# Optimization experiments

Hardware: AMD Instinct MI355X
Metric: run time of the kernel (lower is better)

The kernel has to match this reference:

```python
import jax, jax.numpy as jnp
import numpy as np
import math

B, T, D, CAP = 4, 1024, 512, 32768
MEM_UPDATE_MOMENTUM = 0.99
MEM_NEW_DATA_RATE = 0.01

def setup_inputs() -> dict:
    key = jax.random.key(0)
    k1, k2, k3, k4, k5 = jax.random.split(key, 5)
    keys = jax.random.normal(k1, (B, T, D), dtype=jnp.float32)
    values = jax.random.normal(k2, (B, T, D), dtype=jnp.float32)
    importance = jax.random.uniform(k3, (B, T, 1), dtype=jnp.float32)
    query = jax.random.normal(k4, (B, T, D), dtype=jnp.float32)
    # xavier_uniform on (1, CAP, D): fan_in=D, fan_out=CAP (torch treats dim-1/dim-2)
    bound = math.sqrt(6.0 / (CAP + D))
    mem = jax.random.uniform(k5, (1, CAP, D), minval=-bound, maxval=bound, dtype=jnp.float32)
    return {"keys": keys, "values": values, "importance": importance, "query": query, "mem": mem}

def reference(keys, values, importance, query, mem):
    b, t, d = keys.shape
    cap = mem.shape[1]
    # ---- write ----
    scores = jnp.einsum('btd,ocd->btc', keys, mem)          # [b, t, cap]
    usage = jax.nn.softmax(scores, axis=-1).sum(axis=1)     # [b, cap]
    combined = importance.mean(axis=(1, 2))                 # [b]
    write_priority = combined[:, None] + 0.1 * usage        # [b, cap]
    k = min(t, cap)
    _, indices = jax.lax.top_k(write_priority, k)           # [b, k]
    values_write = values[:, :k]                            # [b, k, d]
    scatter = jnp.zeros((b, cap, d), dtype=keys.dtype)
    scatter = scatter.at[jnp.arange(b)[:, None], indices].set(values_write)
    new_mem = mem * MEM_UPDATE_MOMENTUM + scatter.mean(axis=0, keepdims=True) * MEM_NEW_DATA_RATE
    # ---- read (against updated memory) ----
    attn = jnp.einsum('bqd,ocd->bqc', query, new_mem) / math.sqrt(d)
    attn = jax.nn.softmax(attn, axis=-1)                    # [b, q, cap]
    out = jnp.einsum('bqc,ocd->bqd', attn, new_mem)         # [b, q, d]
    return out
```

## Files before the change

### kernel.cpp

```cpp
#include <hip/hip_runtime.h>

typedef float f32x4 __attribute__((ext_vector_type(4)));
typedef short s16x8 __attribute__((ext_vector_type(8)));
typedef short s16x4 __attribute__((ext_vector_type(4)));
typedef unsigned short ush;

constexpr int Bn = 4, Tn = 1024, Dn = 512, CAPn = 32768, Kn = 1024;
constexpr int ROWS = Bn * Tn;
constexpr float SCALE = 0.044194173824159216f;
constexpr float MOM = 0.99f;
constexpr float RATE_B = 0.0025f;

constexpr size_t OFF_NM    = 0;
constexpr size_t OFF_NMT   = 33554432;
constexpr size_t OFF_OPART = 67108864;
constexpr size_t OFF_KHF   = 67108864;
constexpr size_t OFF_ZPART = 75497472;
constexpr size_t OFF_PRIO  = 83886080;
constexpr size_t OFF_RANK  = 84410368;
constexpr size_t OFF_COMB  = 84934656;
constexpr size_t OFF_ZP2   = 100663296;

#define MFMA(a, b, c) __builtin_amdgcn_mfma_f32_16x16x32_bf16((a), (b), (c), 0, 0, 0)
#define MFMAH(a, b, c) __builtin_amdgcn_mfma_f32_16x16x32_f16((a), (b), (c), 0, 0, 0)

__device__ __forceinline__ ush bfrn(float x) {
  unsigned u = __float_as_uint(x);
  return (ush)((u + 0x7FFFu + ((u >> 16) & 1u)) >> 16);
}
__device__ __forceinline__ float bff(ush h) { return __uint_as_float(((unsigned)h) << 16); }
__device__ __forceinline__ ush f16rn(float x) {
  _Float16 h = (_Float16)x;
  return *(ush*)&h;
}

__device__ __forceinline__ void gl16(const ush* g, ush* l) {
  __builtin_amdgcn_global_load_lds(
      (const __attribute__((address_space(1))) void*)(uintptr_t)g,
      (__attribute__((address_space(3))) void*)(uintptr_t)l, 16, 0, 0);
}

__global__ void k_combined(const float* __restrict__ imp, float* __restrict__ comb) {
  __shared__ float red[256];
  int b = blockIdx.x;
  float s = 0.f;
  for (int t = threadIdx.x; t < Tn; t += 256) s += imp[(size_t)b * Tn + t];
  red[threadIdx.x] = s;
  __syncthreads();
  for (int off = 128; off > 0; off >>= 1) {
    if (threadIdx.x < (unsigned)off) red[threadIdx.x] += red[threadIdx.x + off];
    __syncthreads();
  }
  if (threadIdx.x == 0) comb[b] = red[0] * (1.0f / Tn);
}

__global__ void k_cvt_f16(const float* __restrict__ x, ush* __restrict__ o) {
  size_t i = ((size_t)blockIdx.x * 256 + threadIdx.x) * 4;
  f32x4 v = *(const f32x4*)&x[i];
  s16x4 h;
#pragma unroll
  for (int j = 0; j < 4; ++j) h[j] = (short)f16rn(v[j]);
  *(s16x4*)&o[i] = h;
}

__global__ __launch_bounds__(256, 2) void k_rowexp(const ush* __restrict__ Ahf,
                                                   const ush* __restrict__ Bhf,
                                                   float* __restrict__ zpart) {
  __shared__ ush Bs[64 * 512];
  __shared__ float red[2][64];
  const int tid = threadIdx.x;
  const int lane = tid & 63, wid = tid >> 6;
  const int wc2 = wid >> 1, wt = wid & 1;
  const int l15 = lane & 15, g = lane >> 4;
  const int cb = blockIdx.x;
  const int cBase = cb * 64;

  s16x8 afr[2][16];
#pragma unroll
  for (int mi = 0; mi < 2; ++mi) {
    int c = cBase + wc2 * 32 + mi * 16 + l15;
#pragma unroll
    for (int ks = 0; ks < 16; ++ks)
      afr[mi][ks] = *(const s16x8*)&Ahf[(size_t)c * Dn + ks * 32 + g * 8];
  }

  for (int tt = 0; tt < 64; ++tt) {
    const int tBase = tt * 64;
#pragma unroll
    for (int rr = 0; rr < 16; ++rr) {
      int idx = rr * 256 + tid;
      int row = idx >> 6, ch = idx & 63;
      gl16(&Bhf[(size_t)(tBase + row) * Dn + ((ch ^ (row & 7)) << 3)],
           &Bs[rr * 2048 + wid * 512]);
    }
    __syncthreads();
    f32x4 S[2][2];
#pragma unroll
    for (int mi = 0; mi < 2; ++mi)
#pragma unroll
      for (int ni = 0; ni < 2; ++ni) S[mi][ni] = (f32x4){0.f, 0.f, 0.f, 0.f};
#pragma unroll
    for (int ks = 0; ks < 16; ++ks) {
      s16x8 bfr[2];
#pragma unroll
      for (int ni = 0; ni < 2; ++ni) {
        int trow = wt * 32 + ni * 16 + l15;
        bfr[ni] = *(const s16x8*)&Bs[trow * 512 + (((ks * 4 + g) ^ (trow & 7)) * 8)];
      }
#pragma unroll
      for (int mi = 0; mi < 2; ++mi)
#pragma unroll
        for (int ni = 0; ni < 2; ++ni) S[mi][ni] = MFMAH(afr[mi][ks], bfr[ni], S[mi][ni]);
    }
    float tacc[2] = {0.f, 0.f};
#pragma unroll
    for (int mi = 0; mi < 2; ++mi)
#pragma unroll
      for (int ni = 0; ni < 2; ++ni)
#pragma unroll
        for (int r = 0; r < 4; ++r) tacc[ni] += __expf(S[mi][ni][r]);
#pragma unroll
    for (int ni = 0; ni < 2; ++ni) {
      float v = tacc[ni];
      v += __shfl_xor(v, 16);
      v += __shfl_xor(v, 32);
      tacc[ni] = v;
    }
    if (g == 0) {
      red[wc2][wt * 32 + l15] = tacc[0];
      red[wc2][wt * 32 + 16 + l15] = tacc[1];
    }
    __syncthreads();
    if (tid < 64) zpart[(size_t)cb * ROWS + tBase + tid] = red[0][tid] + red[1][tid];
  }
}

__global__ void k_invl(const float* __restrict__ zpart, float* __restrict__ invl) {
  int t = blockIdx.x * 256 + threadIdx.x;
  float s = 0.f;
  for (int cb = 0; cb < 512; ++cb) s += zpart[(size_t)cb * ROWS + t];
  invl[t] = 1.0f / s;
}

__global__ __launch_bounds__(256, 3) void k_usage(const ush* __restrict__ mhf,
                                                  const ush* __restrict__ khf,
                                                  const float* __restrict__ invl,
                                                  const float* __restrict__ comb,
                                                  float* __restrict__ prio) {
  __shared__ ush Ah[128 * 64], Bh[128 * 64];
  const int tid = threadIdx.x;
  const int lane = tid & 63, w = tid >> 6;
  const int l15 = lane & 15, g = lane >> 4;
  const int cBase = blockIdx.x * 128;
  const int b = blockIdx.y;
  const ush* khb = khf + (size_t)b * Tn * Dn;
  const int r0 = tid >> 3, u0 = tid & 7;
  const int usw = (u0 ^ (r0 & 7)) << 3;

  float uacc[2][4] = {{0.f, 0.f, 0.f, 0.f}, {0.f, 0.f, 0.f, 0.f}};
  for (int tt = 0; tt < 8; ++tt) {
    f32x4 S[2][8];
#pragma unroll
    for (int mi = 0; mi < 2; ++mi)
#pragma unroll
      for (int ni = 0; ni < 8; ++ni) S[mi][ni] = (f32x4){0.f, 0.f, 0.f, 0.f};
    for (int kk = 0; kk < 8; ++kk) {
      __syncthreads();
      {
        size_t a0 = (size_t)(cBase + r0) * Dn + kk * 64 + usw;
        size_t a1 = (size_t)(cBase + r0 + 64) * Dn + kk * 64 + usw;
        gl16(&mhf[a0], &Ah[w * 512]);
        gl16(&mhf[a1], &Ah[4096 + w * 512]);
        size_t b0 = (size_t)(tt * 128 + r0) * Dn + kk * 64 + usw;
        size_t b1 = (size_t)(tt * 128 + r0 + 64) * Dn + kk * 64 + usw;
        gl16(&khb[b0], &Bh[w * 512]);
        gl16(&khb[b1], &Bh[4096 + w * 512]);
      }
      __syncthreads();
#pragma unroll
      for (int ks2 = 0; ks2 < 2; ++ks2) {
        s16x8 ah[2];
#pragma unroll
        for (int mi = 0; mi < 2; ++mi) {
          int crow = w * 32 + mi * 16 + l15;
          ah[mi] = *(const s16x8*)&Ah[crow * 64 + (((ks2 * 4 + g) ^ (crow & 7)) * 8)];
        }
#pragma unroll
        for (int ni = 0; ni < 8; ++ni) {
          int trow = ni * 16 + l15;
          s16x8 bh = *(const s16x8*)&Bh[trow * 64 + (((ks2 * 4 + g) ^ (trow & 7)) * 8)];
#pragma unroll
          for (int mi = 0; mi < 2; ++mi) S[mi][ni] = MFMAH(ah[mi], bh, S[mi][ni]);
        }
      }
    }
#pragma unroll
    for (int ni = 0; ni < 8; ++ni) {
      float il = invl[b * Tn + tt * 128 + ni * 16 + l15];
#pragma unroll
      for (int mi = 0; mi < 2; ++mi)
#pragma unroll
        for (int r = 0; r < 4; ++r) uacc[mi][r] += __expf(S[mi][ni][r]) * il;
    }
  }
#pragma unroll
  for (int mi = 0; mi < 2; ++mi)
#pragma unroll
    for (int r = 0; r < 4; ++r) {
      float v = uacc[mi][r];
      v += __shfl_xor(v, 1);
      v += __shfl_xor(v, 2);
      v += __shfl_xor(v, 4);
      v += __shfl_xor(v, 8);
      if (l15 == 0)
        prio[(size_t)b * CAPn + cBase + w * 32 + mi * 16 + g * 4 + r] =
            comb[b] + 0.1f * v;
    }
}

__global__ void k_rankinit(int* __restrict__ rank) {
  rank[blockIdx.x * 256 + threadIdx.x] = Kn;
}

__global__ __launch_bounds__(1024) void k_select(const float* __restrict__ prio,
                                                 int* __restrict__ rank) {
  const int b = blockIdx.x;
  const float* p = prio + (size_t)b * CAPn;
  __shared__ int hist[256];
  __shared__ unsigned long long s_pref;
  __shared__ int s_krem;
  __shared__ int s_cnt;
  __shared__ unsigned long long selk[Kn];
  const int tid = threadIdx.x;
  if (tid == 0) { s_pref = 0ull; s_krem = Kn; s_cnt = 0; }

#define KEYOF(c, kk)                                                         \
  {                                                                          \
    unsigned mb_ = __float_as_uint(p[(c)]);                                  \
    mb_ = (mb_ & 0x80000000u) ? ~mb_ : (mb_ | 0x80000000u);                  \
    (kk) = ((unsigned long long)mb_ << 32) | (unsigned)(0xFFFFFFFFu - (c));  \
  }

  __syncthreads();
  for (int pos = 56; pos >= 0; pos -= 8) {
    if (tid < 256) hist[tid] = 0;
    __syncthreads();
    unsigned long long pref = s_pref;
    unsigned long long maskhi = (pos == 56) ? 0ull : (~0ull << (pos + 8));
    for (int c = tid; c < CAPn; c += 1024) {
      unsigned long long k;
      KEYOF(c, k);
      if ((k & maskhi) == pref) atomicAdd(&hist[(int)((k >> pos) & 255)], 1);
    }
    __syncthreads();
    if (tid == 0) {
      int krem = s_krem;
      int d = 255;
      for (;; --d) {
        int h = hist[d];
        if (krem <= h || d == 0) break;
        krem -= h;
      }
      s_pref = pref | ((unsigned long long)d << pos);
      s_krem = krem;
    }
    __syncthreads();
  }
  unsigned long long T = s_pref;
  for (int c = tid; c < CAPn; c += 1024) {
    unsigned long long k;
    KEYOF(c, k);
    if (k >= T) {
      int idx = atomicAdd(&s_cnt, 1);
      selk[idx] = k;
    }
  }
  __syncthreads();
  unsigned long long mine = selk[tid];
  int r = 0;
  for (int j = 0; j < Kn; ++j) r += (selk[j] > mine) ? 1 : 0;
  int c = (int)(0xFFFFFFFFu - (unsigned)(mine & 0xFFFFFFFFull));
  rank[(size_t)b * CAPn + c] = r;
#undef KEYOF
}

__global__ void k_newmem(const float* __restrict__ mem, const float* __restrict__ values,
                         const int* __restrict__ rank, ush* __restrict__ nm) {
  int gid = blockIdx.x * 256 + threadIdx.x;
  int c = gid >> 7;
  int q = (gid & 127) << 2;
  f32x4 m = *(const f32x4*)&mem[(size_t)c * Dn + q];
  f32x4 acc = {0.f, 0.f, 0.f, 0.f};
#pragma unroll
  for (int b = 0; b < Bn; ++b) {
    int r = rank[(size_t)b * CAPn + c];
    if (r < Kn) acc += *(const f32x4*)&values[((size_t)b * Tn + r) * Dn + q];
  }
  f32x4 res = m * MOM + acc * RATE_B;
  s16x4 o;
#pragma unroll
  for (int j = 0; j < 4; ++j) o[j] = (short)bfrn(res[j]);
  *(s16x4*)&nm[(size_t)c * Dn + q] = o;
}

__global__ void k_nmT(const ush* __restrict__ nm, ush* __restrict__ nmT) {
  __shared__ ush tile[64][65];
  int cBase = blockIdx.x * 64, dBase = blockIdx.y * 64;
  int tid = threadIdx.x;
#pragma unroll
  for (int rr = 0; rr < 2; ++rr) {
    int idx = rr * 256 + tid;
    int row = idx >> 3, ch = idx & 7;
    s16x8 v = *(const s16x8*)&nm[(size_t)(cBase + row) * Dn + dBase + ch * 8];
#pragma unroll
    for (int j = 0; j < 8; ++j) tile[row][ch * 8 + j] = (ush)v[j];
  }
  __syncthreads();
#pragma unroll
  for (int rr = 0; rr < 2; ++rr) {
    int idx = rr * 256 + tid;
    int drow = idx >> 3, ch = idx & 7;
    s16x8 v;
#pragma unroll
    for (int j = 0; j < 8; ++j) v[j] = (short)tile[ch * 8 + j][drow];
    *(s16x8*)&nmT[(size_t)(dBase + drow) * CAPn + cBase + ch * 8] = v;
  }
}

#define WAITV2 asm volatile("s_waitcnt vmcnt(2)" ::: "memory")
#define WAITL0 asm volatile("s_waitcnt lgkmcnt(0)" ::: "memory")
#define BAR __builtin_amdgcn_s_barrier()
__global__ __launch_bounds__(512, 1) void k_attnout(
    const float* __restrict__ query, const ush* __restrict__ nm,
    const ush* __restrict__ nmT, ush* __restrict__ opart,
    float* __restrict__ zp2) {
  __shared__ ush lds[65536];
  __shared__ float zred[128];
  __shared__ float zacc[128];
  constexpr int LMS = 0, LMT = 24576, LPS = 49152;
  const int tid = threadIdx.x;
  const int lane = tid & 63, w = tid >> 6;
  const int l15 = lane & 15, g = lane >> 4;
  const int cy = blockIdx.x;
  const int qBase = blockIdx.y * 128;
  const int q = w * 16 + l15;
  const int r0 = tid >> 3, u0 = tid & 7;
  const int usw = (u0 ^ (r0 & 7)) << 3;

  auto stage_ms = [&](int buf, int cb_, int kk) {
    const ush* src = nm + (size_t)cb_ * Dn + kk * 64;
    gl16(&src[(size_t)r0 * Dn + usw], &lds[LMS + buf * 8192 + w * 512]);
    gl16(&src[(size_t)(r0 + 64) * Dn + usw], &lds[LMS + buf * 8192 + 4096 + w * 512]);
  };
  auto stage_mt = [&](int buf, int cb_, int u) {
    const ush* src = nmT + (size_t)((u >> 1) * 128) * CAPn + cb_ + (u & 1) * 64;
    gl16(&src[(size_t)r0 * CAPn + usw], &lds[LMT + buf * 8192 + w * 512]);
    gl16(&src[(size_t)(r0 + 64) * CAPn + usw], &lds[LMT + buf * 8192 + 4096 + w * 512]);
  };

  s16x8 qfr[16];
  {
    const float* qsrc = query + (size_t)(qBase + q) * Dn;
#pragma unroll
    for (int ks = 0; ks < 16; ++ks) {
      f32x4 a = *(const f32x4*)&qsrc[ks * 32 + g * 8];
      f32x4 b = *(const f32x4*)&qsrc[ks * 32 + g * 8 + 4];
      s16x8 h;
#pragma unroll
      for (int j = 0; j < 4; ++j) {
        h[j] = (short)bfrn(a[j]);
        h[4 + j] = (short)bfrn(b[j]);
      }
      qfr[ks] = h;
    }
  }

  f32x4 O[32];
#pragma unroll
  for (int i = 0; i < 32; ++i) O[i] = (f32x4){0.f, 0.f, 0.f, 0.f};
  if (tid < 128) zacc[tid] = 0.f;

  stage_ms(0, cy * 4096, 0);
  stage_ms(1, cy * 4096, 1);

  for (int ct = 0; ct < 32; ++ct) {
    const int cBase = cy * 4096 + ct * 128;
    const int cNext = cy * 4096 + ((ct + 1) & 31) * 128;

    f32x4 S[8];
#pragma unroll
    for (int i = 0; i < 8; ++i) S[i] = (f32x4){0.f, 0.f, 0.f, 0.f};
#pragma unroll
    for (int kk = 0; kk < 8; ++kk) {
      WAITV2;
      WAITL0;
      BAR;
      if (kk < 6) stage_ms((kk + 2) % 3, cBase, kk + 2);
      else if (kk == 6) stage_mt(0, cBase, 0);
      else stage_mt(1, cBase, 1);
      __builtin_amdgcn_s_setprio(1);
#pragma unroll
      for (int ks2 = 0; ks2 < 2; ++ks2) {
#pragma unroll
        for (int mi = 0; mi < 8; ++mi) {
          int row = mi * 16 + l15;
          s16x8 am = *(const s16x8*)&lds[LMS + (kk % 3) * 8192 + row * 64 +
                                         (((ks2 * 4 + g) ^ (row & 7)) << 3)];
          S[mi] = MFMA(am, qfr[kk * 2 + ks2], S[mi]);
        }
      }
      __builtin_amdgcn_s_setprio(0);
    }

    float zl = 0.f;
#pragma unroll
    for (int mi = 0; mi < 8; ++mi) {
      s16x4 p;
#pragma unroll
      for (int r = 0; r < 4; ++r) {
        float e = __expf(S[mi][r] * SCALE);
        zl += e;
        p[r] = (short)bfrn(e);
      }
      int u16 = (mi * 2 + (g >> 1)) ^ l15;
      *(s16x4*)&lds[LPS + q * 128 + u16 * 8 + (g & 1) * 4] = p;
    }
    zl += __shfl_xor(zl, 16);
    zl += __shfl_xor(zl, 32);
    if (g == 0) zred[q] = zl;
    WAITL0;
    BAR;
    if (tid < 128) zacc[tid] += zred[tid];

#pragma unroll
    for (int u = 0; u < 8; ++u) {
      WAITV2;
      WAITL0;
      BAR;
      if (u < 6) stage_mt((u + 2) % 3, cBase, u + 2);
      else if (u == 6) stage_ms(0, cNext, 0);
      else stage_ms(1, cNext, 1);
      __builtin_amdgcn_s_setprio(1);
      const int hh = u & 1;
#pragma unroll
      for (int kc = 0; kc < 2; ++kc) {
        int u16 = (hh * 8 + kc * 4 + g) ^ l15;
        s16x8 pb = *(const s16x8*)&lds[LPS + q * 128 + u16 * 8];
#pragma unroll
        for (int mi = 0; mi < 8; ++mi) {
          int row = mi * 16 + l15;
          s16x8 am = *(const s16x8*)&lds[LMT + (u % 3) * 8192 + row * 64 +
                                         (((kc * 4 + g) ^ (row & 7)) << 3)];
          O[(u >> 1) * 8 + mi] = MFMA(am, pb, O[(u >> 1) * 8 + mi]);
        }
      }
      __builtin_amdgcn_s_setprio(0);
    }
  }

  __syncthreads();
  if (tid < 128) zp2[(size_t)cy * ROWS + qBase + tid] = zacc[tid];
#pragma unroll
  for (int ds = 0; ds < 4; ++ds) {
    __syncthreads();
#pragma unroll
    for (int mi = 0; mi < 8; ++mi) {
      s16x4 ov;
#pragma unroll
      for (int r = 0; r < 4; ++r) ov[r] = (short)bfrn(O[ds * 8 + mi][r]);
      int u16 = (mi * 2 + (g >> 1)) ^ l15;
      *(s16x4*)&lds[LPS + q * 128 + u16 * 8 + (g & 1) * 4] = ov;
    }
    __syncthreads();
#pragma unroll
    for (int i = 0; i < 4; ++i) {
      int slot = i * 512 + tid;
      int qq = slot >> 4, u16 = slot & 15;
      s16x8 v = *(const s16x8*)&lds[LPS + qq * 128 + ((u16 ^ (qq & 15)) << 3)];
      *(s16x8*)&opart[((size_t)cy * ROWS + qBase + qq) * Dn + ds * 128 + u16 * 8] = v;
    }
  }
}

__global__ void k_merge(const ush* __restrict__ opart, const float* __restrict__ zp2,
                        float* __restrict__ out) {
  size_t i = ((size_t)blockIdx.x * 256 + threadIdx.x) * 4;
  int row = (int)(i >> 9);
  float z = 0.f;
#pragma unroll
  for (int cyy = 0; cyy < 8; ++cyy) z += zp2[(size_t)cyy * ROWS + row];
  float inv = 1.0f / z;
  f32x4 acc = {0.f, 0.f, 0.f, 0.f};
#pragma unroll
  for (int cyy = 0; cyy < 8; ++cyy) {
    s16x4 a = *(const s16x4*)&opart[(size_t)cyy * ROWS * Dn + i];
#pragma unroll
    for (int j = 0; j < 4; ++j) acc[j] += bff((ush)a[j]);
  }
#pragma unroll
  for (int j = 0; j < 4; ++j) acc[j] *= inv;
  *(f32x4*)&out[i] = acc;
}

extern "C" void kernel_launch(void* const* d_in, const int* in_sizes, int n_in,
                              void* d_out, int out_size, void* d_ws, size_t ws_size,
                              hipStream_t stream) {
  const float* keys = (const float*)d_in[0];
  const float* values = (const float*)d_in[1];
  const float* importance = (const float*)d_in[2];
  const float* query = (const float*)d_in[3];
  const float* mem = (const float*)d_in[4];
  char* wsb = (char*)d_ws;
  ush* nm    = (ush*)(wsb + OFF_NM);
  ush* nmT   = (ush*)(wsb + OFF_NMT);
  ush* mhf   = (ush*)(wsb + OFF_NMT);
  ush* khf   = (ush*)(wsb + OFF_KHF);
  ush* opart = (ush*)(wsb + OFF_OPART);
  float* zpart = (float*)(wsb + OFF_ZPART);
  float* prio  = (float*)(wsb + OFF_PRIO);
  int* rank    = (int*)(wsb + OFF_RANK);
  float* comb  = (float*)(wsb + OFF_COMB);
  float* zp2   = (float*)(wsb + OFF_ZP2);
  float* invl1 = (float*)(wsb + OFF_COMB + 64);
  float* out = (float*)d_out;

  k_combined<<<Bn, 256, 0, stream>>>(importance, comb);
  k_cvt_f16<<<(ROWS * Dn / 4) / 256, 256, 0, stream>>>(keys, khf);
  k_cvt_f16<<<(CAPn * Dn / 4) / 256, 256, 0, stream>>>(mem, mhf);
  k_rowexp<<<CAPn / 64, 256, 0, stream>>>(mhf, khf, zpart);
  k_invl<<<ROWS / 256, 256, 0, stream>>>(zpart, invl1);
  k_usage<<<dim3(CAPn / 128, Bn), 256, 0, stream>>>(mhf, khf, invl1, comb, prio);
  k_rankinit<<<(Bn * CAPn) / 256, 256, 0, stream>>>(rank);
  k_select<<<Bn, 1024, 0, stream>>>(prio, rank);
  k_newmem<<<(CAPn * Dn / 4) / 256, 256, 0, stream>>>(mem, values, rank, nm);
  k_nmT<<<dim3(CAPn / 64, Dn / 64), 256, 0, stream>>>(nm, nmT);
  k_attnout<<<dim3(8, ROWS / 128), 512, 0, stream>>>(query, nm, nmT, opart, zp2);
  k_merge<<<(ROWS * Dn / 4) / 256, 256, 0, stream>>>(opart, zp2, out);
}
```

Before: 959.3 us.

## Use FP8 for the read-score GEMM and fuse new-memory build into transpose

```diff
diff --git a/kernel.cpp b/kernel.cpp
--- a/kernel.cpp
+++ b/kernel.cpp
@@ -1,17 +1,20 @@
 #include <hip/hip_runtime.h>
+#include <hip/hip_fp8.h>
 
 typedef float f32x4 __attribute__((ext_vector_type(4)));
 typedef short s16x8 __attribute__((ext_vector_type(8)));
 typedef short s16x4 __attribute__((ext_vector_type(4)));
 typedef unsigned short ush;
+typedef unsigned char u8;
 
 constexpr int Bn = 4, Tn = 1024, Dn = 512, CAPn = 32768, Kn = 1024;
 constexpr int ROWS = Bn * Tn;
 constexpr float SCALE = 0.044194173824159216f;
+constexpr float SC64 = SCALE / 64.0f;
 constexpr float MOM = 0.99f;
 constexpr float RATE_B = 0.0025f;
 
-constexpr size_t OFF_NM    = 0;
+constexpr size_t OFF_NM8   = 0;
 constexpr size_t OFF_NMT   = 33554432;
 constexpr size_t OFF_OPART = 67108864;
 constexpr size_t OFF_KHF   = 67108864;
@@ -23,6 +26,7 @@
 
 #define MFMA(a, b, c) __builtin_amdgcn_mfma_f32_16x16x32_bf16((a), (b), (c), 0, 0, 0)
 #define MFMAH(a, b, c) __builtin_amdgcn_mfma_f32_16x16x32_f16((a), (b), (c), 0, 0, 0)
+#define MFMA8(a, b, c) __builtin_amdgcn_mfma_f32_16x16x32_fp8_fp8((a), (b), (c), 0, 0, 0)
 
 __device__ __forceinline__ ush bfrn(float x) {
   unsigned u = __float_as_uint(x);
@@ -33,8 +37,12 @@
   _Float16 h = (_Float16)x;
   return *(ush*)&h;
 }
-
-__device__ __forceinline__ void gl16(const ush* g, ush* l) {
+__device__ __forceinline__ u8 f8rn(float x) {
+  __hip_fp8_e4m3 v(x);
+  return (u8)v.__x;
+}
+
+__device__ __forceinline__ void gl16(const void* g, void* l) {
   __builtin_amdgcn_global_load_lds(
       (const __attribute__((address_space(1))) void*)(uintptr_t)g,
       (__attribute__((address_space(3))) void*)(uintptr_t)l, 16, 0, 0);
@@ -284,8 +292,8 @@
 #undef KEYOF
 }
 
-__global__ void k_newmem(const float* __restrict__ mem, const float* __restrict__ values,
-                         const int* __restrict__ rank, ush* __restrict__ nm) {
+__global__ void k_newmem8(const float* __restrict__ mem, const float* __restrict__ values,
+                          const int* __restrict__ rank, u8* __restrict__ nm8) {
   int gid = blockIdx.x * 256 + threadIdx.x;
   int c = gid >> 7;
   int q = (gid & 127) << 2;
@@ -296,34 +304,44 @@
     int r = rank[(size_t)b * CAPn + c];
     if (r < Kn) acc += *(const f32x4*)&values[((size_t)b * Tn + r) * Dn + q];
   }
-  f32x4 res = m * MOM + acc * RATE_B;
-  s16x4 o;
-#pragma unroll
-  for (int j = 0; j < 4; ++j) o[j] = (short)bfrn(res[j]);
-  *(s16x4*)&nm[(size_t)c * Dn + q] = o;
-}
-
-__global__ void k_nmT(const ush* __restrict__ nm, ush* __restrict__ nmT) {
+  f32x4 res = (m * MOM + acc * RATE_B) * 64.0f;
+  union { u8 b[4]; unsigned w; } out;
+#pragma unroll
+  for (int j = 0; j < 4; ++j) out.b[j] = f8rn(res[j]);
+  *(unsigned*)&nm8[(size_t)c * Dn + q] = out.w;
+}
+
+__global__ __launch_bounds__(256) void k_nmT(const float* __restrict__ mem,
+                                             const float* __restrict__ values,
+                                             const int* __restrict__ rank,
+                                             ush* __restrict__ nmT) {
   __shared__ ush tile[64][65];
   int cBase = blockIdx.x * 64, dBase = blockIdx.y * 64;
   int tid = threadIdx.x;
-#pragma unroll
-  for (int rr = 0; rr < 2; ++rr) {
-    int idx = rr * 256 + tid;
-    int row = idx >> 3, ch = idx & 7;
-    s16x8 v = *(const s16x8*)&nm[(size_t)(cBase + row) * Dn + dBase + ch * 8];
-#pragma unroll
-    for (int j = 0; j < 8; ++j) tile[row][ch * 8 + j] = (ush)v[j];
+  int c = tid >> 2, dq = (tid & 3) * 16;
+  int rr[4];
+#pragma unroll
+  for (int b = 0; b < Bn; ++b) rr[b] = rank[(size_t)b * CAPn + cBase + c];
+#pragma unroll
+  for (int j = 0; j < 4; ++j) {
+    f32x4 m = *(const f32x4*)&mem[(size_t)(cBase + c) * Dn + dBase + dq + j * 4];
+    f32x4 a = {0.f, 0.f, 0.f, 0.f};
+#pragma unroll
+    for (int b = 0; b < Bn; ++b)
+      if (rr[b] < Kn)
+        a += *(const f32x4*)&values[((size_t)b * Tn + rr[b]) * Dn + dBase + dq + j * 4];
+    f32x4 res = m * MOM + a * RATE_B;
+#pragma unroll
+    for (int jj = 0; jj < 4; ++jj) tile[c][dq + j * 4 + jj] = bfrn(res[jj]);
   }
   __syncthreads();
-#pragma unroll
-  for (int rr = 0; rr < 2; ++rr) {
-    int idx = rr * 256 + tid;
-    int drow = idx >> 3, ch = idx & 7;
+  int drow = tid >> 2, cq = (tid & 3) * 16;
+#pragma unroll
+  for (int k = 0; k < 2; ++k) {
     s16x8 v;
 #pragma unroll
-    for (int j = 0; j < 8; ++j) v[j] = (short)tile[ch * 8 + j][drow];
-    *(s16x8*)&nmT[(size_t)(dBase + drow) * CAPn + cBase + ch * 8] = v;
+    for (int j = 0; j < 8; ++j) v[j] = (short)tile[cq + k * 8 + j][drow];
+    *(s16x8*)&nmT[(size_t)(dBase + drow) * CAPn + cBase + cq + k * 8] = v;
   }
 }
 
@@ -331,13 +349,13 @@
 #define WAITL0 asm volatile("s_waitcnt lgkmcnt(0)" ::: "memory")
 #define BAR __builtin_amdgcn_s_barrier()
 __global__ __launch_bounds__(512, 1) void k_attnout(
-    const float* __restrict__ query, const ush* __restrict__ nm,
+    const float* __restrict__ query, const u8* __restrict__ nm8,
     const ush* __restrict__ nmT, ush* __restrict__ opart,
     float* __restrict__ zp2) {
-  __shared__ ush lds[65536];
+  __shared__ __align__(16) u8 L[131072];
   __shared__ float zred[128];
   __shared__ float zacc[128];
-  constexpr int LMS = 0, LMT = 24576, LPS = 49152;
+  constexpr int LMS = 0, LMT = 49152, LPS = 98304;
   const int tid = threadIdx.x;
   const int lane = tid & 63, w = tid >> 6;
   const int l15 = lane & 15, g = lane >> 4;
@@ -346,32 +364,33 @@
   const int q = w * 16 + l15;
   const int r0 = tid >> 3, u0 = tid & 7;
   const int usw = (u0 ^ (r0 & 7)) << 3;
+  const int usw8 = (u0 ^ (r0 & 7)) << 4;
 
   auto stage_ms = [&](int buf, int cb_, int kk) {
-    const ush* src = nm + (size_t)cb_ * Dn + kk * 64;
-    gl16(&src[(size_t)r0 * Dn + usw], &lds[LMS + buf * 8192 + w * 512]);
-    gl16(&src[(size_t)(r0 + 64) * Dn + usw], &lds[LMS + buf * 8192 + 4096 + w * 512]);
+    const u8* src = nm8 + (size_t)cb_ * Dn + kk * 128;
+    gl16(&src[(size_t)r0 * Dn + usw8], &L[LMS + buf * 16384 + w * 1024]);
+    gl16(&src[(size_t)(r0 + 64) * Dn + usw8], &L[LMS + buf * 16384 + 8192 + w * 1024]);
   };
   auto stage_mt = [&](int buf, int cb_, int u) {
     const ush* src = nmT + (size_t)((u >> 1) * 128) * CAPn + cb_ + (u & 1) * 64;
-    gl16(&src[(size_t)r0 * CAPn + usw], &lds[LMT + buf * 8192 + w * 512]);
-    gl16(&src[(size_t)(r0 + 64) * CAPn + usw], &lds[LMT + buf * 8192 + 4096 + w * 512]);
+    gl16(&src[(size_t)r0 * CAPn + usw], &L[LMT + buf * 16384 + w * 1024]);
+    gl16(&src[(size_t)(r0 + 64) * CAPn + usw], &L[LMT + buf * 16384 + 8192 + w * 1024]);
   };
 
-  s16x8 qfr[16];
+  long qfr8[16];
   {
     const float* qsrc = query + (size_t)(qBase + q) * Dn;
 #pragma unroll
     for (int ks = 0; ks < 16; ++ks) {
       f32x4 a = *(const f32x4*)&qsrc[ks * 32 + g * 8];
       f32x4 b = *(const f32x4*)&qsrc[ks * 32 + g * 8 + 4];
-      s16x8 h;
+      union { u8 c[8]; long l; } u;
 #pragma unroll
       for (int j = 0; j < 4; ++j) {
-        h[j] = (short)bfrn(a[j]);
-        h[4 + j] = (short)bfrn(b[j]);
-      }
-      qfr[ks] = h;
+        u.c[j] = f8rn(a[j]);
+        u.c[4 + j] = f8rn(b[j]);
+      }
+      qfr8[ks] = u.l;
     }
   }
 
@@ -391,22 +410,23 @@
 #pragma unroll
     for (int i = 0; i < 8; ++i) S[i] = (f32x4){0.f, 0.f, 0.f, 0.f};
 #pragma unroll
-    for (int kk = 0; kk < 8; ++kk) {
+    for (int kk = 0; kk < 4; ++kk) {
       WAITV2;
       WAITL0;
       BAR;
-      if (kk < 6) stage_ms((kk + 2) % 3, cBase, kk + 2);
-      else if (kk == 6) stage_mt(0, cBase, 0);
+      if (kk < 2) stage_ms((kk + 2) % 3, cBase, kk + 2);
+      else if (kk == 2) stage_mt(0, cBase, 0);
       else stage_mt(1, cBase, 1);
       __builtin_amdgcn_s_setprio(1);
 #pragma unroll
-      for (int ks2 = 0; ks2 < 2; ++ks2) {
+      for (int ks = 0; ks < 4; ++ks) {
 #pragma unroll
         for (int mi = 0; mi < 8; ++mi) {
           int row = mi * 16 + l15;
-          s16x8 am = *(const s16x8*)&lds[LMS + (kk % 3) * 8192 + row * 64 +
-                                         (((ks2 * 4 + g) ^ (row & 7)) << 3)];
-          S[mi] = MFMA(am, qfr[kk * 2 + ks2], S[mi]);
+          long a = *(const long*)&L[LMS + (kk % 3) * 16384 + row * 128 +
+                                    (((ks * 2 + (g >> 1)) ^ (row & 7)) << 4) +
+                                    (g & 1) * 8];
+          S[mi] = MFMA8(a, qfr8[kk * 4 + ks], S[mi]);
         }
       }
       __builtin_amdgcn_s_setprio(0);
@@ -418,12 +438,12 @@
       s16x4 p;
 #pragma unroll
       for (int r = 0; r < 4; ++r) {
-        float e = __expf(S[mi][r] * SCALE);
+        float e = __expf(S[mi][r] * SC64);
         zl += e;
         p[r] = (short)bfrn(e);
       }
       int u16 = (mi * 2 + (g >> 1)) ^ l15;
-      *(s16x4*)&lds[LPS + q * 128 + u16 * 8 + (g & 1) * 4] = p;
+      *(s16x4*)&L[LPS + q * 256 + u16 * 16 + (g & 1) * 8] = p;
     }
     zl += __shfl_xor(zl, 16);
     zl += __shfl_xor(zl, 32);
@@ -445,12 +465,12 @@
 #pragma unroll
       for (int kc = 0; kc < 2; ++kc) {
         int u16 = (hh * 8 + kc * 4 + g) ^ l15;
-        s16x8 pb = *(const s16x8*)&lds[LPS + q * 128 + u16 * 8];
+        s16x8 pb = *(const s16x8*)&L[LPS + q * 256 + u16 * 16];
 #pragma unroll
         for (int mi = 0; mi < 8; ++mi) {
           int row = mi * 16 + l15;
-          s16x8 am = *(const s16x8*)&lds[LMT + (u % 3) * 8192 + row * 64 +
-                                         (((kc * 4 + g) ^ (row & 7)) << 3)];
+          s16x8 am = *(const s16x8*)&L[LMT + (u % 3) * 16384 + row * 128 +
+                                       (((kc * 4 + g) ^ (row & 7)) << 4)];
           O[(u >> 1) * 8 + mi] = MFMA(am, pb, O[(u >> 1) * 8 + mi]);
         }
       }
@@ -469,14 +489,14 @@
 #pragma unroll
       for (int r = 0; r < 4; ++r) ov[r] = (short)bfrn(O[ds * 8 + mi][r]);
       int u16 = (mi * 2 + (g >> 1)) ^ l15;
-      *(s16x4*)&lds[LPS + q * 128 + u16 * 8 + (g & 1) * 4] = ov;
+      *(s16x4*)&L[LPS + q * 256 + u16 * 16 + (g & 1) * 8] = ov;
     }
     __syncthreads();
 #pragma unroll
     for (int i = 0; i < 4; ++i) {
       int slot = i * 512 + tid;
       int qq = slot >> 4, u16 = slot & 15;
-      s16x8 v = *(const s16x8*)&lds[LPS + qq * 128 + ((u16 ^ (qq & 15)) << 3)];
+      s16x8 v = *(const s16x8*)&L[LPS + qq * 256 + ((u16 ^ (qq & 15)) << 4)];
       *(s16x8*)&opart[((size_t)cy * ROWS + qBase + qq) * Dn + ds * 128 + u16 * 8] = v;
     }
   }
@@ -511,7 +531,7 @@
   const float* query = (const float*)d_in[3];
   const float* mem = (const float*)d_in[4];
   char* wsb = (char*)d_ws;
-  ush* nm    = (ush*)(wsb + OFF_NM);
+  u8* nm8    = (u8*)(wsb + OFF_NM8);
   ush* nmT   = (ush*)(wsb + OFF_NMT);
   ush* mhf   = (ush*)(wsb + OFF_NMT);
   ush* khf   = (ush*)(wsb + OFF_KHF);
@@ -532,8 +552,8 @@
   k_usage<<<dim3(CAPn / 128, Bn), 256, 0, stream>>>(mhf, khf, invl1, comb, prio);
   k_rankinit<<<(Bn * CAPn) / 256, 256, 0, stream>>>(rank);
   k_select<<<Bn, 1024, 0, stream>>>(prio, rank);
-  k_newmem<<<(CAPn * Dn / 4) / 256, 256, 0, stream>>>(mem, values, rank, nm);
-  k_nmT<<<dim3(CAPn / 64, Dn / 64), 256, 0, stream>>>(nm, nmT);
-  k_attnout<<<dim3(8, ROWS / 128), 512, 0, stream>>>(query, nm, nmT, opart, zp2);
+  k_newmem8<<<(CAPn * Dn / 4) / 256, 256, 0, stream>>>(mem, values, rank, nm8);
+  k_nmT<<<dim3(CAPn / 64, Dn / 64), 256, 0, stream>>>(mem, values, rank, nmT);
+  k_attnout<<<dim3(8, ROWS / 128), 512, 0, stream>>>(query, nm8, nmT, opart, zp2);
   k_merge<<<(ROWS * Dn / 4) / 256, 256, 0, stream>>>(opart, zp2, out);
 }
```

Measured after the change: 857.4 us. -10.6%, faster.
